# Optimization experiments

Measured on AMD Instinct MI355X. Metric: run time of the kernel, lower is better.

## Reference

```python
import jax, jax.numpy as jnp
import numpy as np
from jax import lax

N, R, W, H = 256, 32, 8, 6       # batch, n_rooms, room width/height
MX, MY = 72, 72                  # map grid
EMB = 6                          # room embedding width
CIN = 10 + EMB                   # conv input channels


def _boundaries(m):
    # m: [R, W, H] binary room masks -> [R, 4, W, H] (left, right, up, down edges)
    left = jnp.concatenate([m[:, :1, :], jnp.clip(m[:, 1:, :] - m[:, :-1, :], 0)], axis=1)
    right = jnp.concatenate([jnp.clip(m[:, :-1, :] - m[:, 1:, :], 0), m[:, -1:, :]], axis=1)
    up = jnp.concatenate([m[:, :, :1], jnp.clip(m[:, :, 1:] - m[:, :, :-1], 0)], axis=2)
    down = jnp.concatenate([jnp.clip(m[:, :, :-1] - m[:, :, 1:], 0), m[:, :, -1:]], axis=2)
    return jnp.stack([left, right, up, down], axis=1)


def setup_inputs() -> dict:
    key = jax.random.key(0)
    ks = jax.random.split(key, 12)
    room_map = (jax.random.uniform(ks[0], (R, W, H)) < 0.7).astype(jnp.float32)
    room_map = room_map.at[:, 0, 0].set(1.0)  # guarantee nonempty rooms
    doors = (jax.random.uniform(ks[1], (R, 4, W, H)) < 0.15).astype(jnp.float32) * room_map[:, None]
    room_tensor = jnp.concatenate([room_map[:, None], doors, _boundaries(room_map)], axis=1)  # [R,9,W,H]
    px = jax.random.randint(ks[2], (N, R), 0, MX - W)
    py = jax.random.randint(ks[3], (N, R), 0, MY - H)
    room_positions = jnp.stack([px, py], axis=-1).astype(jnp.int32)  # [N,R,2]

    def rn(k, shape, fan_in):
        return jax.random.normal(k, shape, jnp.float32) / np.float32(np.sqrt(fan_in))

    inp = dict(room_positions=room_positions, room_tensor=room_tensor)
    inp['room_embedding'] = jax.random.normal(ks[4], (R, EMB), jnp.float32)
    inp['w_conv1'] = rn(ks[5], (64, CIN, 5, 5), CIN * 25); inp['b_conv1'] = jnp.zeros((64,), jnp.float32)
    inp['w_conv2'] = rn(ks[6], (64, 64, 3, 3), 64 * 9);    inp['b_conv2'] = jnp.zeros((64,), jnp.float32)
    inp['w_conv3'] = rn(ks[7], (64, 64, 3, 3), 64 * 9);    inp['b_conv3'] = jnp.zeros((64,), jnp.float32)
    inp['w_room1'] = rn(ks[8], (128, 64), 64);   inp['b_room1'] = jnp.zeros((128,), jnp.float32)
    inp['w_room2'] = rn(ks[9], (128, 128), 128); inp['b_room2'] = jnp.zeros((128,), jnp.float32)
    inp['w_fc1'] = rn(ks[10], (256, 128), 128);  inp['b_fc1'] = jnp.zeros((256,), jnp.float32)
    inp['w_fc2'] = rn(ks[11], (256, 256), 256);  inp['b_fc2'] = jnp.zeros((256,), jnp.float32)
    return inp


def _conv2d_relu(x, w, b):
    pad = w.shape[-1] // 2
    y = lax.conv_general_dilated(x, w, (1, 1), [(pad, pad), (pad, pad)],
                                 dimension_numbers=('NCHW', 'OIHW', 'NCHW'))
    return jax.nn.relu(y + b[None, :, None, None])


def _forward(room_positions, room_tensor, room_embedding,
             w_conv1, b_conv1, w_conv2, b_conv2, w_conv3, b_conv3,
             w_room1, b_room1, w_room2, b_room2, w_fc1, b_fc1, w_fc2, b_fc2):
    room_map = room_tensor[:, 0]                      # [R,W,H]
    px = room_positions[..., 0]                       # [N,R]
    py = room_positions[..., 1]
    # ---- encode_map: scatter-add all rooms into grid ----
    bidx = jnp.arange(N)[:, None, None, None, None]
    cidx = jnp.arange(9)[None, None, :, None, None]
    ix = px[:, :, None, None, None] + jnp.arange(W)[None, None, None, :, None]   # [N,R,1,W,1]
    iy = py[:, :, None, None, None] + jnp.arange(H)[None, None, None, None, :]   # [N,R,1,1,H]
    map9 = jnp.zeros((N, 9, MX, MY), jnp.float32).at[bidx, cidx, ix, iy].add(room_tensor[None])
    eidx = jnp.arange(EMB)[None, None, :, None, None]
    evals = room_embedding[:, :, None, None] * room_map[:, None, :, :]           # [R,EMB,W,H]
    embg = jnp.zeros((N, EMB, MX, MY), jnp.float32).at[bidx, eidx, ix, iy].add(evals[None])
    X = jnp.concatenate([map9, jnp.ones((N, 1, MX, MY), jnp.float32), embg], axis=1)  # [N,16,MX,MY]
    # ---- map convs ----
    X = _conv2d_relu(X, w_conv1, b_conv1)
    X = _conv2d_relu(X, w_conv2, b_conv2)
    X = _conv2d_relu(X, w_conv3, b_conv3)
    # ---- decode_map: gather room tiles, masked mean per room ----
    Xt = jnp.transpose(X, (0, 2, 3, 1))                                          # [N,MX,MY,C]
    g = Xt[jnp.arange(N)[:, None, None, None],
           px[:, :, None, None] + jnp.arange(W)[None, None, :, None],
           py[:, :, None, None] + jnp.arange(H)[None, None, None, :]]            # [N,R,W,H,C]
    g = g * room_map[None, :, :, :, None]
    room_feat = g.sum(axis=(2, 3)) / room_map.sum(axis=(1, 2))[None, :, None]    # [N,R,C]
    X = jnp.transpose(room_feat, (0, 2, 1))                                      # [N,C,R]
    # ---- 1x1 conv1d room layers ----
    X = jax.nn.relu(jnp.einsum('ncr,oc->nor', X, w_room1) + b_room1[None, :, None])
    X = jax.nn.relu(jnp.einsum('ncr,oc->nor', X, w_room2) + b_room2[None, :, None])
    # ---- fc head: sum over rooms, MLP ----
    X = X.sum(axis=2)                                                            # [N,128]
    X = jax.nn.relu(X @ w_fc1.T + b_fc1)
    return X @ w_fc2.T + b_fc2                                                   # [N,256]


def reference(room_positions, room_tensor, room_embedding,
              w_conv1, b_conv1, w_conv2, b_conv2, w_conv3, b_conv3,
              w_room1, b_room1, w_room2, b_room2, w_fc1, b_fc1, w_fc2, b_fc2):
    return _forward(room_positions, room_tensor, room_embedding,
                    w_conv1, b_conv1, w_conv2, b_conv2, w_conv3, b_conv3,
                    w_room1, b_room1, w_room2, b_room2, w_fc1, b_fc1, w_fc2, b_fc2)
```

## Files before the change

kernel.cpp:

```cpp
#include <hip/hip_runtime.h>
#include <hip/hip_bf16.h>
#include <cstddef>

#define NB 256
#define RR 32
#define WW 8
#define HH 6
#define MXY 72
#define EMB 6
#define CIN1 16

typedef __bf16 bf16x8 __attribute__((ext_vector_type(8)));
typedef float floatx4 __attribute__((ext_vector_type(4)));

static const size_t B_W1F  = 0;
static const size_t B_W2F  = 57344;
static const size_t B_W3F  = 131072;
static const size_t B_RAUX = 204800;
static const size_t B_RINV = 205056;
static const size_t B_HEAD = 205312;
static const size_t F_WR1T = 0;
static const size_t F_WR2T = 8192;
static const size_t F_F1T  = 24576;
static const size_t F_F2T  = 57344;
static const size_t B_FEAT = 696832;
static const size_t B_IMSK = 2793984;
static const size_t B_SSUM = 2826752;

__device__ inline short f2b(float f) {
    unsigned u = __builtin_bit_cast(unsigned, f);
    unsigned r = (u + 0x7fffu + ((u >> 16) & 1u)) >> 16;
    return (short)r;
}

__global__ void prep_all(const float* __restrict__ w1, const float* __restrict__ w2,
                         const float* __restrict__ w3, const float* __restrict__ wr1,
                         const float* __restrict__ wr2, const float* __restrict__ wf1,
                         const float* __restrict__ wf2, const float* __restrict__ rt,
                         const int* __restrict__ pos, char* __restrict__ ws)
{
    short* W1F = (short*)(ws + B_W1F);
    short* W2F = (short*)(ws + B_W2F);
    short* W3F = (short*)(ws + B_W3F);
    float* HEAD = (float*)(ws + B_HEAD);

    int idx = blockIdx.x * 256 + threadIdx.x;
    if (idx < 28672) {
        int j = idx & 7, lane = (idx >> 3) & 63, nt = (idx >> 9) & 3, kk = idx >> 11;
        int k = kk * 32 + (lane >> 4) * 8 + j;
        int oc = nt * 16 + (lane & 15);
        int tap = k >> 4, ci = k & 15;
        float v = (tap < 25) ? w1[(oc * 16 + ci) * 25 + tap] : 0.f;
        W1F[idx] = f2b(v);
        return;
    }
    idx -= 28672;
    if (idx < 36864) {
        int j = idx & 7, lane = (idx >> 3) & 63, nt = (idx >> 9) & 3, kk = idx >> 11;
        int k = kk * 32 + (lane >> 4) * 8 + j;
        int oc = nt * 16 + (lane & 15);
        int tap = k >> 6, cp = k & 63;
        int ci = (cp >> 2) + (cp & 3) * 16;
        W2F[idx] = f2b(w2[(oc * 64 + ci) * 9 + tap]);
        return;
    }
    idx -= 36864;
    if (idx < 36864) {
        int j = idx & 7, lane = (idx >> 3) & 63, nt = (idx >> 9) & 3, kk = idx >> 11;
        int k = kk * 32 + (lane >> 4) * 8 + j;
        int oc = nt * 16 + (lane & 15);
        int tap = k >> 6, cp = k & 63;
        int ci = (cp >> 2) + (cp & 3) * 16;
        W3F[idx] = f2b(w3[(oc * 64 + ci) * 9 + tap]);
        return;
    }
    idx -= 36864;
    if (idx < 8192)  { int o = idx & 127, c = idx >> 7; HEAD[F_WR1T + idx] = wr1[o * 64 + c]; return; }
    idx -= 8192;
    if (idx < 16384) { int o = idx & 127, c = idx >> 7; HEAD[F_WR2T + idx] = wr2[o * 128 + c]; return; }
    idx -= 16384;
    if (idx < 32768) { int o = idx & 255, c = idx >> 8; HEAD[F_F1T + idx] = wf1[o * 128 + c]; return; }
    idx -= 32768;
    if (idx < 65536) { int o = idx & 255, c = idx >> 8; HEAD[F_F2T + idx] = wf2[o * 256 + c]; return; }
    idx -= 65536;
    if (idx < 8192) {
        const int n = idx >> 5, r0 = idx & 31;
        const int px0 = pos[(n * RR + r0) * 2 + 0];
        const int py0 = pos[(n * RR + r0) * 2 + 1];
        unsigned m = 0;
        for (int r = 0; r < RR; ++r) {
            int rpx = pos[(n * RR + r) * 2 + 0];
            int rpy = pos[(n * RR + r) * 2 + 1];
            if (rpx >= px0 - 11 && rpx <= px0 + 11 && rpy >= py0 - 9 && rpy <= py0 + 9)
                m |= 1u << r;
        }
        ((unsigned*)(ws + B_IMSK))[n * RR + r0] = m;
        return;
    }
    idx -= 8192;
    if (idx < RR) {
        unsigned long long m = 0ull;
        int cnt = 0;
        for (int j = 0; j < WW * HH; ++j)
            if (rt[idx * 9 * 48 + j] != 0.f) { m |= (1ull << j); ++cnt; }
        ((unsigned long long*)(ws + B_RAUX))[idx] = m;
        ((float*)(ws + B_RINV))[idx] = 1.f / (float)cnt;
    }
}

__global__ __launch_bounds__(256, 4) void fused_conv(
    const unsigned* __restrict__ imask, const float* __restrict__ rt,
    const float* __restrict__ emb, const short* __restrict__ wAll,
    const float* __restrict__ bc1, const float* __restrict__ bc2,
    const float* __restrict__ bc3, const int* __restrict__ pos,
    const unsigned long long* __restrict__ rmask, float* __restrict__ feat)
{
    __shared__ __align__(16) short s_Y1[120 * 72];
    __shared__ __align__(16) short s_u[80 * 72];
    __shared__ __align__(16) short s_B[2][2048];
    __shared__ float s_feat[64];

    const int tid = threadIdx.x;
    const int lane = tid & 63;
    const int wv = tid >> 6;
    const int ml = lane & 15;
    const int q = lane >> 4;
    const int room = blockIdx.x;
    const int n = blockIdx.y;

    const int px = pos[(n * RR + room) * 2 + 0];
    const int py = pos[(n * RR + room) * 2 + 1];

    const char* wB = (const char*)wAll;
    auto dma = [&](int k) {
        const char* src = wB + (size_t)k * 4096 + wv * 1024 + lane * 16;
        __builtin_amdgcn_global_load_lds(
            (const __attribute__((address_space(1))) unsigned int*)src,
            (__attribute__((address_space(3))) unsigned int*)&s_B[k & 1][wv * 512],
            16, 0, 0);
    };

    dma(0);

    {
        const unsigned mk0 = imask[n * RR + room];
        if (tid < 224) {
            const int row = tid / 14, col = tid - (tid / 14) * 14;
            const int gx = px - 4 + row, gy = py - 4 + col;
            float a[16];
#pragma unroll
            for (int c = 0; c < 16; ++c) a[c] = 0.f;
            a[9] = ((unsigned)gx < (unsigned)MXY && (unsigned)gy < (unsigned)MXY) ? 1.f : 0.f;

            unsigned mm = mk0;
            while (mm) {
                const int r = __builtin_ctz(mm);
                mm &= mm - 1;
                const int rpx = pos[(n * RR + r) * 2 + 0];
                const int rpy = pos[(n * RR + r) * 2 + 1];
                const int w = gx - rpx, h = gy - rpy;
                if ((unsigned)w < (unsigned)WW && (unsigned)h < (unsigned)HH) {
                    const int j = w * HH + h;
                    const float* rr = rt + r * 9 * 48;
#pragma unroll
                    for (int c = 0; c < 9; ++c) a[c] += rr[c * 48 + j];
                    const float mv = rr[j];
#pragma unroll
                    for (int e = 0; e < EMB; ++e) a[10 + e] += emb[r * EMB + e] * mv;
                }
            }
            short o[16];
#pragma unroll
            for (int c = 0; c < 16; ++c) o[c] = f2b(a[c]);
            *reinterpret_cast<uint4*>(&s_u[tid * 24 + 0]) = *reinterpret_cast<uint4*>(o);
            *reinterpret_cast<uint4*>(&s_u[tid * 24 + 8]) = *reinterpret_cast<uint4*>(o + 8);
        }
    }
    __syncthreads();

    {
        int prow[2], pcol[2];
#pragma unroll
        for (int i = 0; i < 2; ++i) {
            int p = wv * 32 + i * 16 + ml;
            if (p > 119) p = 119;
            prow[i] = p / 10; pcol[i] = p - prow[i] * 10;
        }
        floatx4 acc1[2][4] = {};

#pragma unroll
        for (int k = 0; k < 14; ++k) {
            dma(k + 1);
            const short* sb = s_B[k & 1];
            bf16x8 Bf[4];
#pragma unroll
            for (int j2 = 0; j2 < 4; ++j2)
                Bf[j2] = *reinterpret_cast<const bf16x8*>(&sb[(j2 * 64 + lane) * 8]);
            int tap = k * 2 + (q >> 1);
            if (tap > 24) tap = 24;
            const int chb = (q & 1) * 8;
            const int dx = tap / 5, dy = tap - (tap / 5) * 5;
            __builtin_amdgcn_s_setprio(1);
#pragma unroll
            for (int i = 0; i < 2; ++i) {
                bf16x8 A = *reinterpret_cast<const bf16x8*>(
                    &s_u[((prow[i] + dx) * 14 + (pcol[i] + dy)) * 24 + chb]);
#pragma unroll
                for (int j2 = 0; j2 < 4; ++j2)
                    acc1[i][j2] = __builtin_amdgcn_mfma_f32_16x16x32_bf16(
                        A, Bf[j2], acc1[i][j2], 0, 0, 0);
            }
            __builtin_amdgcn_s_setprio(0);
            if (k == 13) {
                float b4[4];
#pragma unroll
                for (int j2 = 0; j2 < 4; ++j2) b4[j2] = bc1[j2 * 16 + ml];
#pragma unroll
                for (int i = 0; i < 2; ++i)
#pragma unroll
                    for (int r = 0; r < 4; ++r) {
                        int p = wv * 32 + i * 16 + q * 4 + r;
                        if (p < 120) {
                            unsigned lo = (unsigned)(unsigned short)f2b(fmaxf(acc1[i][0][r] + b4[0], 0.f))
                                        | ((unsigned)(unsigned short)f2b(fmaxf(acc1[i][1][r] + b4[1], 0.f)) << 16);
                            unsigned hi = (unsigned)(unsigned short)f2b(fmaxf(acc1[i][2][r] + b4[2], 0.f))
                                        | ((unsigned)(unsigned short)f2b(fmaxf(acc1[i][3][r] + b4[3], 0.f)) << 16);
                            *reinterpret_cast<uint2*>(&s_Y1[p * 72 + ml * 4]) = make_uint2(lo, hi);
                        }
                    }
            }
            __syncthreads();
        }
    }

    {
        int prowA, pcolA, prowB, pcolB;
        {
            int p0 = wv * 16 + ml; prowA = p0 >> 3; pcolA = p0 & 7;
            int p1 = 64 + ml;      prowB = p1 >> 3; pcolB = p1 & 7;
        }
        floatx4 acc2[4] = {};
        floatx4 acc2s = {};

#pragma unroll
        for (int k = 14; k < 32; ++k) {
            dma(k + 1);
            const short* sb = s_B[k & 1];
            const int kk = k - 14;
            bf16x8 Bf[4];
#pragma unroll
            for (int j2 = 0; j2 < 4; ++j2)
                Bf[j2] = *reinterpret_cast<const bf16x8*>(&sb[(j2 * 64 + lane) * 8]);
            bf16x8 B4 = *reinterpret_cast<const bf16x8*>(&sb[(wv * 64 + lane) * 8]);
            const int tap = kk >> 1;
            const int chb = (kk & 1) * 32 + q * 8;
            const int dx = tap / 3, dy = tap - (tap / 3) * 3;
            bf16x8 A0 = *reinterpret_cast<const bf16x8*>(
                &s_Y1[((prowA + dx) * 10 + (pcolA + dy)) * 72 + chb]);
            bf16x8 A4 = *reinterpret_cast<const bf16x8*>(
                &s_Y1[((prowB + dx) * 10 + (pcolB + dy)) * 72 + chb]);
            __builtin_amdgcn_s_setprio(1);
#pragma unroll
            for (int j2 = 0; j2 < 4; ++j2)
                acc2[j2] = __builtin_amdgcn_mfma_f32_16x16x32_bf16(A0, Bf[j2], acc2[j2], 0, 0, 0);
            acc2s = __builtin_amdgcn_mfma_f32_16x16x32_bf16(A4, B4, acc2s, 0, 0, 0);
            __builtin_amdgcn_s_setprio(0);
            if (k == 31) {
                float b4[4];
#pragma unroll
                for (int j2 = 0; j2 < 4; ++j2) b4[j2] = bc2[j2 * 16 + ml];
#pragma unroll
                for (int r = 0; r < 4; ++r) {
                    int p = wv * 16 + q * 4 + r;
                    unsigned lo = (unsigned)(unsigned short)f2b(fmaxf(acc2[0][r] + b4[0], 0.f))
                                | ((unsigned)(unsigned short)f2b(fmaxf(acc2[1][r] + b4[1], 0.f)) << 16);
                    unsigned hi = (unsigned)(unsigned short)f2b(fmaxf(acc2[2][r] + b4[2], 0.f))
                                | ((unsigned)(unsigned short)f2b(fmaxf(acc2[3][r] + b4[3], 0.f)) << 16);
                    *reinterpret_cast<uint2*>(&s_u[p * 72 + ml * 4]) = make_uint2(lo, hi);
                }
                float bt = bc2[wv * 16 + ml];
#pragma unroll
                for (int r = 0; r < 4; ++r) {
                    int p = 64 + q * 4 + r;
                    s_u[p * 72 + ml * 4 + wv] = f2b(fmaxf(acc2s[r] + bt, 0.f));
                }
                if (tid < 64) s_feat[tid] = 0.f;
            }
            __syncthreads();
        }
    }

    {
        int prow3, pcol3;
        {
            int p0 = wv * 16 + ml;
            prow3 = p0 / 6; pcol3 = p0 - (p0 / 6) * 6;
        }
        floatx4 acc3[4] = {};

#pragma unroll
        for (int k = 32; k < 50; ++k) {
            if (k + 1 < 50) dma(k + 1);
            const short* sb = s_B[k & 1];
            const int kk = k - 32;
            if (wv < 3) {
                bf16x8 Bf[4];
#pragma unroll
                for (int j2 = 0; j2 < 4; ++j2)
                    Bf[j2] = *reinterpret_cast<const bf16x8*>(&sb[(j2 * 64 + lane) * 8]);
                const int tap = kk >> 1;
                const int chb = (kk & 1) * 32 + q * 8;
                const int dx = tap / 3, dy = tap - (tap / 3) * 3;
                bf16x8 A = *reinterpret_cast<const bf16x8*>(
                    &s_u[((prow3 + dx) * 8 + (pcol3 + dy)) * 72 + chb]);
                __builtin_amdgcn_s_setprio(1);
#pragma unroll
                for (int j2 = 0; j2 < 4; ++j2)
                    acc3[j2] = __builtin_amdgcn_mfma_f32_16x16x32_bf16(A, Bf[j2], acc3[j2], 0, 0, 0);
                __builtin_amdgcn_s_setprio(0);
            }
            if (k == 49 && wv < 3) {
                float b4[4];
#pragma unroll
                for (int j2 = 0; j2 < 4; ++j2) b4[j2] = bc3[j2 * 16 + ml];
                float part[4] = {0.f, 0.f, 0.f, 0.f};
                const unsigned long long mk = rmask[room];
#pragma unroll
                for (int r = 0; r < 4; ++r) {
                    int p = wv * 16 + q * 4 + r;
                    if ((mk >> p) & 1ull) {
#pragma unroll
                        for (int j2 = 0; j2 < 4; ++j2)
                            part[j2] += fmaxf(acc3[j2][r] + b4[j2], 0.f);
                    }
                }
#pragma unroll
                for (int j2 = 0; j2 < 4; ++j2) {
                    part[j2] += __shfl_xor(part[j2], 16);
                    part[j2] += __shfl_xor(part[j2], 32);
                }
                if (q == 0) {
#pragma unroll
                    for (int j2 = 0; j2 < 4; ++j2)
                        atomicAdd(&s_feat[j2 * 16 + ml], part[j2]);
                }
            }
            __syncthreads();
        }
    }

    if (tid < 64)
        feat[((size_t)n * RR + room) * 64 + tid] = s_feat[tid];
}

__global__ __launch_bounds__(256) void head_rooms(const float* __restrict__ feat,
                                                  const float* __restrict__ HEAD,
                                                  const float* __restrict__ rinv,
                                                  const float* __restrict__ b1,
                                                  const float* __restrict__ b2,
                                                  float* __restrict__ ssum)
{
    __shared__ __align__(16) float s_feat[8 * 64];
    __shared__ __align__(16) float s_h1[8 * 128];
    __shared__ __align__(16) float s_s[2 * 128];

    const int qr = blockIdx.x;
    const int n = blockIdx.y;
    const int tid = threadIdx.x;
    const float* W1t = HEAD + F_WR1T;
    const float* W2t = HEAD + F_WR2T;

    for (int i = tid; i < 8 * 64; i += 256)
        s_feat[i] = feat[(size_t)n * RR * 64 + qr * 512 + i] * rinv[qr * 8 + (i >> 6)];
    __syncthreads();

    const int o = tid & 127;
    const int rh = tid >> 7;

    float acc[4];
#pragma unroll
    for (int r = 0; r < 4; ++r) acc[r] = b1[o];
    for (int c4 = 0; c4 < 16; ++c4) {
        float w0 = W1t[(c4 * 4 + 0) * 128 + o];
        float w1 = W1t[(c4 * 4 + 1) * 128 + o];
        float w2 = W1t[(c4 * 4 + 2) * 128 + o];
        float w3 = W1t[(c4 * 4 + 3) * 128 + o];
#pragma unroll
        for (int r = 0; r < 4; ++r) {
            float4 f = *reinterpret_cast<const float4*>(&s_feat[(rh * 4 + r) * 64 + c4 * 4]);
            acc[r] += f.x * w0 + f.y * w1 + f.z * w2 + f.w * w3;
        }
    }
#pragma unroll
    for (int r = 0; r < 4; ++r) s_h1[(rh * 4 + r) * 128 + o] = fmaxf(acc[r], 0.f);
    __syncthreads();

#pragma unroll
    for (int r = 0; r < 4; ++r) acc[r] = b2[o];
    for (int c4 = 0; c4 < 32; ++c4) {
        float w0 = W2t[(c4 * 4 + 0) * 128 + o];
        float w1 = W2t[(c4 * 4 + 1) * 128 + o];
        float w2 = W2t[(c4 * 4 + 2) * 128 + o];
        float w3 = W2t[(c4 * 4 + 3) * 128 + o];
#pragma unroll
        for (int r = 0; r < 4; ++r) {
            float4 f = *reinterpret_cast<const float4*>(&s_h1[(rh * 4 + r) * 128 + c4 * 4]);
            acc[r] += f.x * w0 + f.y * w1 + f.z * w2 + f.w * w3;
        }
    }
    float ps = 0.f;
#pragma unroll
    for (int r = 0; r < 4; ++r) ps += fmaxf(acc[r], 0.f);
    s_s[rh * 128 + o] = ps;
    __syncthreads();
    if (tid < 128)
        ssum[((size_t)n * 4 + qr) * 128 + tid] = s_s[tid] + s_s[128 + tid];
}

__global__ __launch_bounds__(256) void head_fc(const float* __restrict__ ssum,
                                               const float* __restrict__ HEAD,
                                               const float* __restrict__ bf1,
                                               const float* __restrict__ bf2,
                                               float* __restrict__ outp)
{
    __shared__ __align__(16) float s_sf[128];
    __shared__ __align__(16) float s_t1[256];

    const int n = blockIdx.x;
    const int tid = threadIdx.x;
    const float* F1t = HEAD + F_F1T;
    const float* F2t = HEAD + F_F2T;

    if (tid < 128) {
        const float* s0 = ssum + (size_t)n * 4 * 128 + tid;
        s_sf[tid] = (s0[0] + s0[128]) + (s0[256] + s0[384]);
    }
    __syncthreads();

    {
        float a = bf1[tid];
#pragma unroll 4
        for (int c4 = 0; c4 < 32; ++c4) {
            float4 f = *reinterpret_cast<const float4*>(&s_sf[c4 * 4]);
            a += f.x * F1t[(c4 * 4 + 0) * 256 + tid];
            a += f.y * F1t[(c4 * 4 + 1) * 256 + tid];
            a += f.z * F1t[(c4 * 4 + 2) * 256 + tid];
            a += f.w * F1t[(c4 * 4 + 3) * 256 + tid];
        }
        s_t1[tid] = fmaxf(a, 0.f);
    }
    __syncthreads();

    {
        float a = bf2[tid];
#pragma unroll 4
        for (int c4 = 0; c4 < 64; ++c4) {
            float4 f = *reinterpret_cast<const float4*>(&s_t1[c4 * 4]);
            a += f.x * F2t[(c4 * 4 + 0) * 256 + tid];
            a += f.y * F2t[(c4 * 4 + 1) * 256 + tid];
            a += f.z * F2t[(c4 * 4 + 2) * 256 + tid];
            a += f.w * F2t[(c4 * 4 + 3) * 256 + tid];
        }
        outp[(size_t)n * 256 + tid] = a;
    }
}

extern "C" void kernel_launch(void* const* d_in, const int* in_sizes, int n_in,
                              void* d_out, int out_size, void* d_ws, size_t ws_size,
                              hipStream_t stream)
{
    const int* pos = (const int*)d_in[0];
    const float* rt = (const float*)d_in[1];
    const float* emb = (const float*)d_in[2];
    const float* w1 = (const float*)d_in[3];
    const float* bc1 = (const float*)d_in[4];
    const float* w2 = (const float*)d_in[5];
    const float* bc2 = (const float*)d_in[6];
    const float* w3 = (const float*)d_in[7];
    const float* bc3 = (const float*)d_in[8];
    const float* wr1 = (const float*)d_in[9];
    const float* br1 = (const float*)d_in[10];
    const float* wr2 = (const float*)d_in[11];
    const float* br2 = (const float*)d_in[12];
    const float* wf1 = (const float*)d_in[13];
    const float* bf1 = (const float*)d_in[14];
    const float* wf2 = (const float*)d_in[15];
    const float* bf2 = (const float*)d_in[16];
    float* out = (float*)d_out;
    char* ws = (char*)d_ws;

    prep_all<<<913, 256, 0, stream>>>(w1, w2, w3, wr1, wr2, wf1, wf2, rt, pos, ws);

    const short* WALL = (const short*)(ws + B_W1F);
    const unsigned long long* RMASK = (const unsigned long long*)(ws + B_RAUX);
    const float* RINV = (const float*)(ws + B_RINV);
    const float* HEAD = (const float*)(ws + B_HEAD);
    float* FEAT = (float*)(ws + B_FEAT);
    unsigned* IMSK = (unsigned*)(ws + B_IMSK);
    float* SSUM = (float*)(ws + B_SSUM);

    fused_conv<<<dim3(RR, NB), 256, 0, stream>>>(IMSK, rt, emb, WALL,
                                                 bc1, bc2, bc3, pos, RMASK, FEAT);

    head_rooms<<<dim3(4, NB), 256, 0, stream>>>(FEAT, HEAD, RINV, br1, br2, SSUM);
    head_fc<<<NB, 256, 0, stream>>>(SSUM, HEAD, bf1, bf2, out);
}
```

Before: 272.2 us.

## Trim padded conv1 K-step and split conv3 output channels across all four waves

Conv1's K dimension is shrunk from 14 to 13 steps of 32, dropping a step that held only zero-padded taps, and the weight buffer offsets and prep grid are adjusted to match. Conv3 now gives each of the four waves one 16-channel output slice across all three 16-pixel tiles, where before three waves each did one pixel tile with all 64 channels and the fourth sat idle. Each wave therefore writes its own s_feat slice directly, which removes the shared-memory atomics and the s_feat zeroing. The risk lies in the workspace layout and the pipeline step indices, which must stay consistent with the dma() staging.

New measurement: 268.5 us. No clear change (-1.4%).

```diff
diff --git a/kernel.cpp b/kernel.cpp
--- a/kernel.cpp
+++ b/kernel.cpp
@@ -14,8 +14,8 @@
 typedef float floatx4 __attribute__((ext_vector_type(4)));
 
 static const size_t B_W1F  = 0;
-static const size_t B_W2F  = 57344;
-static const size_t B_W3F  = 131072;
+static const size_t B_W2F  = 53248;
+static const size_t B_W3F  = 126976;
 static const size_t B_RAUX = 204800;
 static const size_t B_RINV = 205056;
 static const size_t B_HEAD = 205312;
@@ -45,7 +45,7 @@
     float* HEAD = (float*)(ws + B_HEAD);
 
     int idx = blockIdx.x * 256 + threadIdx.x;
-    if (idx < 28672) {
+    if (idx < 26624) {
         int j = idx & 7, lane = (idx >> 3) & 63, nt = (idx >> 9) & 3, kk = idx >> 11;
         int k = kk * 32 + (lane >> 4) * 8 + j;
         int oc = nt * 16 + (lane & 15);
@@ -54,7 +54,7 @@
         W1F[idx] = f2b(v);
         return;
     }
-    idx -= 28672;
+    idx -= 26624;
     if (idx < 36864) {
         int j = idx & 7, lane = (idx >> 3) & 63, nt = (idx >> 9) & 3, kk = idx >> 11;
         int k = kk * 32 + (lane >> 4) * 8 + j;
@@ -189,7 +189,7 @@
         floatx4 acc1[2][4] = {};
 
 #pragma unroll
-        for (int k = 0; k < 14; ++k) {
+        for (int k = 0; k < 13; ++k) {
             dma(k + 1);
             const short* sb = s_B[k & 1];
             bf16x8 Bf[4];
@@ -211,7 +211,7 @@
                         A, Bf[j2], acc1[i][j2], 0, 0, 0);
             }
             __builtin_amdgcn_s_setprio(0);
-            if (k == 13) {
+            if (k == 12) {
                 float b4[4];
 #pragma unroll
                 for (int j2 = 0; j2 < 4; ++j2) b4[j2] = bc1[j2 * 16 + ml];
@@ -243,10 +243,10 @@
         floatx4 acc2s = {};
 
 #pragma unroll
-        for (int k = 14; k < 32; ++k) {
+        for (int k = 13; k < 31; ++k) {
             dma(k + 1);
             const short* sb = s_B[k & 1];
-            const int kk = k - 14;
+            const int kk = k - 13;
             bf16x8 Bf[4];
 #pragma unroll
             for (int j2 = 0; j2 < 4; ++j2)
@@ -265,7 +265,7 @@
                 acc2[j2] = __builtin_amdgcn_mfma_f32_16x16x32_bf16(A0, Bf[j2], acc2[j2], 0, 0, 0);
             acc2s = __builtin_amdgcn_mfma_f32_16x16x32_bf16(A4, B4, acc2s, 0, 0, 0);
             __builtin_amdgcn_s_setprio(0);
-            if (k == 31) {
+            if (k == 30) {
                 float b4[4];
 #pragma unroll
                 for (int j2 = 0; j2 < 4; ++j2) b4[j2] = bc2[j2 * 16 + ml];
@@ -284,66 +284,52 @@
                     int p = 64 + q * 4 + r;
                     s_u[p * 72 + ml * 4 + wv] = f2b(fmaxf(acc2s[r] + bt, 0.f));
                 }
-                if (tid < 64) s_feat[tid] = 0.f;
             }
             __syncthreads();
         }
     }
 
     {
-        int prow3, pcol3;
-        {
-            int p0 = wv * 16 + ml;
-            prow3 = p0 / 6; pcol3 = p0 - (p0 / 6) * 6;
-        }
-        floatx4 acc3[4] = {};
-
-#pragma unroll
-        for (int k = 32; k < 50; ++k) {
-            if (k + 1 < 50) dma(k + 1);
+        int prow3[3], pcol3[3];
+#pragma unroll
+        for (int i = 0; i < 3; ++i) {
+            int p = i * 16 + ml;
+            prow3[i] = p / 6; pcol3[i] = p - (p / 6) * 6;
+        }
+        floatx4 acc3[3] = {};
+
+#pragma unroll
+        for (int k = 31; k < 49; ++k) {
+            if (k + 1 < 49) dma(k + 1);
             const short* sb = s_B[k & 1];
-            const int kk = k - 32;
-            if (wv < 3) {
-                bf16x8 Bf[4];
-#pragma unroll
-                for (int j2 = 0; j2 < 4; ++j2)
-                    Bf[j2] = *reinterpret_cast<const bf16x8*>(&sb[(j2 * 64 + lane) * 8]);
-                const int tap = kk >> 1;
-                const int chb = (kk & 1) * 32 + q * 8;
-                const int dx = tap / 3, dy = tap - (tap / 3) * 3;
+            const int kk = k - 31;
+            bf16x8 Bf = *reinterpret_cast<const bf16x8*>(&sb[(wv * 64 + lane) * 8]);
+            const int tap = kk >> 1;
+            const int chb = (kk & 1) * 32 + q * 8;
+            const int dx = tap / 3, dy = tap - (tap / 3) * 3;
+            __builtin_amdgcn_s_setprio(1);
+#pragma unroll
+            for (int i = 0; i < 3; ++i) {
                 bf16x8 A = *reinterpret_cast<const bf16x8*>(
-                    &s_u[((prow3 + dx) * 8 + (pcol3 + dy)) * 72 + chb]);
-                __builtin_amdgcn_s_setprio(1);
-#pragma unroll
-                for (int j2 = 0; j2 < 4; ++j2)
-                    acc3[j2] = __builtin_amdgcn_mfma_f32_16x16x32_bf16(A, Bf[j2], acc3[j2], 0, 0, 0);
-                __builtin_amdgcn_s_setprio(0);
-            }
-            if (k == 49 && wv < 3) {
-                float b4[4];
-#pragma unroll
-                for (int j2 = 0; j2 < 4; ++j2) b4[j2] = bc3[j2 * 16 + ml];
-                float part[4] = {0.f, 0.f, 0.f, 0.f};
+                    &s_u[((prow3[i] + dx) * 8 + (pcol3[i] + dy)) * 72 + chb]);
+                acc3[i] = __builtin_amdgcn_mfma_f32_16x16x32_bf16(A, Bf, acc3[i], 0, 0, 0);
+            }
+            __builtin_amdgcn_s_setprio(0);
+            if (k == 48) {
+                const float bt = bc3[wv * 16 + ml];
+                float part = 0.f;
                 const unsigned long long mk = rmask[room];
 #pragma unroll
-                for (int r = 0; r < 4; ++r) {
-                    int p = wv * 16 + q * 4 + r;
-                    if ((mk >> p) & 1ull) {
-#pragma unroll
-                        for (int j2 = 0; j2 < 4; ++j2)
-                            part[j2] += fmaxf(acc3[j2][r] + b4[j2], 0.f);
+                for (int i = 0; i < 3; ++i)
+#pragma unroll
+                    for (int r = 0; r < 4; ++r) {
+                        int p = i * 16 + q * 4 + r;
+                        if ((mk >> p) & 1ull)
+                            part += fmaxf(acc3[i][r] + bt, 0.f);
                     }
-                }
-#pragma unroll
-                for (int j2 = 0; j2 < 4; ++j2) {
-                    part[j2] += __shfl_xor(part[j2], 16);
-                    part[j2] += __shfl_xor(part[j2], 32);
-                }
-                if (q == 0) {
-#pragma unroll
-                    for (int j2 = 0; j2 < 4; ++j2)
-                        atomicAdd(&s_feat[j2 * 16 + ml], part[j2]);
-                }
+                part += __shfl_xor(part, 16);
+                part += __shfl_xor(part, 32);
+                if (q == 0) s_feat[wv * 16 + ml] = part;
             }
             __syncthreads();
         }
@@ -489,7 +475,7 @@
     float* out = (float*)d_out;
     char* ws = (char*)d_ws;
 
-    prep_all<<<913, 256, 0, stream>>>(w1, w2, w3, wr1, wr2, wf1, wf2, rt, pos, ws);
+    prep_all<<<905, 256, 0, stream>>>(w1, w2, w3, wr1, wr2, wf1, wf2, rt, pos, ws);
 
     const short* WALL = (const short*)(ws + B_W1F);
     const unsigned long long* RMASK = (const unsigned long long*)(ws + B_RAUX);
```
